# Kernel optimization log

Measured on AMD Instinct MI355X. Metric: run time of the kernel, lower is better.

The kernel has to match this reference:

```python
import jax, jax.numpy as jnp
import numpy as np

DIM = 192
HEADS = 6
HEAD_DIM = DIM // HEADS
WS = (7, 7, 7)
SHIFT = (3, 3, 3)
RES = (14, 56, 56)
MLP_HIDDEN = DIM * 4
N = WS[0] * WS[1] * WS[2]  # 343 tokens per window
SCALE = HEAD_DIM ** (-0.5)


def _rel_pos_index():
    coords = np.stack(np.meshgrid(np.arange(WS[0]), np.arange(WS[1]), np.arange(WS[2]), indexing='ij'))
    cf = coords.reshape(3, -1)  # (3, N)
    rel = (cf[:, :, None] - cf[:, None, :]).transpose(1, 2, 0).astype(np.int64)  # (N, N, 3)
    rel[..., 0] += WS[0] - 1
    rel[..., 1] += WS[1] - 1
    rel[..., 2] += WS[2] - 1
    rel[..., 0] *= (2 * WS[1] - 1) * (2 * WS[2] - 1)
    rel[..., 1] *= 2 * WS[2] - 1
    return rel.sum(-1)  # (N, N)


def _attn_mask():
    S, H, W = RES
    img = np.zeros((S, H, W), dtype=np.float32)
    cnt = 0
    for s in (slice(0, -WS[0]), slice(-WS[0], -SHIFT[0]), slice(-SHIFT[0], None)):
        for h in (slice(0, -WS[1]), slice(-WS[1], -SHIFT[1]), slice(-SHIFT[1], None)):
            for w in (slice(0, -WS[2]), slice(-WS[2], -SHIFT[2]), slice(-SHIFT[2], None)):
                img[s, h, w] = cnt
                cnt += 1
    m = img.reshape(S // WS[0], WS[0], H // WS[1], WS[1], W // WS[2], WS[2])
    m = m.transpose(0, 2, 4, 1, 3, 5).reshape(-1, N)  # (nW, N)
    diff = m[:, None, :] - m[:, :, None]
    return np.where(diff != 0, -100.0, 0.0).astype(np.float32)  # (nW, N, N)


REL_IDX = jnp.asarray(_rel_pos_index())
ATTN_MASK = jnp.asarray(_attn_mask())


def _window_partition(x):
    # x: (B, S, H, W, C) -> (B*nW, N, C)
    B, S, H, W, C = x.shape
    x = x.reshape(B, S // WS[0], WS[0], H // WS[1], WS[1], W // WS[2], WS[2], C)
    x = x.transpose(0, 1, 3, 5, 2, 4, 6, 7)
    return x.reshape(-1, N, C)


def _window_reverse(wins, B):
    S, H, W = RES
    C = wins.shape[-1]
    x = wins.reshape(B, S // WS[0], H // WS[1], W // WS[2], WS[0], WS[1], WS[2], C)
    x = x.transpose(0, 1, 4, 2, 5, 3, 6, 7)
    return x.reshape(B, S, H, W, C)


def _layernorm(x, g, b):
    mu = x.mean(-1, keepdims=True)
    var = ((x - mu) ** 2).mean(-1, keepdims=True)
    return (x - mu) * jax.lax.rsqrt(var + 1e-5) * g + b


def setup_inputs() -> dict:
    key = jax.random.key(0)
    ks = jax.random.split(key, 16)
    p = lambda k, shape, s=0.02: (jax.random.normal(k, shape, dtype=jnp.float32) * s)
    return {
        'x': jax.random.normal(ks[0], (1, DIM) + RES, dtype=jnp.float32),
        'norm1_g': jnp.ones((DIM,), jnp.float32),
        'norm1_b': jnp.zeros((DIM,), jnp.float32),
        'qkv_w': p(ks[1], (DIM, 3 * DIM)),
        'qkv_b': jnp.zeros((3 * DIM,), jnp.float32),
        'rpb_table': p(ks[2], ((2 * WS[0] - 1) * (2 * WS[1] - 1) * (2 * WS[2] - 1), HEADS)),
        'proj_w': p(ks[3], (DIM, DIM)),
        'proj_b': jnp.zeros((DIM,), jnp.float32),
        'norm2_g': jnp.ones((DIM,), jnp.float32),
        'norm2_b': jnp.zeros((DIM,), jnp.float32),
        'fc1_w': p(ks[4], (DIM, MLP_HIDDEN)),
        'fc1_b': jnp.zeros((MLP_HIDDEN,), jnp.float32),
        'fc2_w': p(ks[5], (MLP_HIDDEN, DIM)),
        'fc2_b': jnp.zeros((DIM,), jnp.float32),
    }


def reference(x, norm1_g, norm1_b, qkv_w, qkv_b, rpb_table, proj_w, proj_b,
              norm2_g, norm2_b, fc1_w, fc1_b, fc2_w, fc2_b):
    B, C, S, H, W = x.shape
    L = S * H * W
    xt = x.transpose(0, 2, 3, 4, 1).reshape(B, L, C)  # b (s h w) c
    shortcut = xt
    xn = _layernorm(xt, norm1_g, norm1_b).reshape(B, S, H, W, C)
    xs = jnp.roll(xn, (-SHIFT[0], -SHIFT[1], -SHIFT[2]), axis=(1, 2, 3))
    xw = _window_partition(xs)  # (B*nW, N, C)
    B_ = xw.shape[0]
    nW = B_ // B

    qkv = (xw @ qkv_w + qkv_b).reshape(B_, N, 3, HEADS, HEAD_DIM)
    q = qkv[:, :, 0].transpose(0, 2, 1, 3) * SCALE  # (B_, h, N, d)
    k = qkv[:, :, 1].transpose(0, 2, 1, 3)
    v = qkv[:, :, 2].transpose(0, 2, 1, 3)

    attn = jnp.einsum('bhnd,bhmd->bhnm', q, k)
    bias = rpb_table[REL_IDX.reshape(-1)].reshape(N, N, HEADS).transpose(2, 0, 1)  # (h, N, N)
    attn = attn + bias[None]
    attn = attn.reshape(B, nW, HEADS, N, N) + ATTN_MASK[None, :, None]
    attn = jax.nn.softmax(attn.reshape(B_, HEADS, N, N), axis=-1)

    out = jnp.einsum('bhnm,bhmd->bhnd', attn, v).transpose(0, 2, 1, 3).reshape(B_, N, C)
    out = out @ proj_w + proj_b

    xr = _window_reverse(out, B)
    xr = jnp.roll(xr, (SHIFT[0], SHIFT[1], SHIFT[2]), axis=(1, 2, 3)).reshape(B, L, C)
    xt = shortcut + xr

    h = _layernorm(xt, norm2_g, norm2_b)
    h = jax.nn.gelu(h @ fc1_w + fc1_b, approximate=False) @ fc2_w + fc2_b
    xt = xt + h

    return xt.reshape(B, S, H, W, C).transpose(0, 4, 1, 2, 3)  # (B, C, S, H, W)
```

## Files before the change

kernel.cpp:

```cpp
#include <hip/hip_runtime.h>
#include <hip/hip_bf16.h>
#include <math.h>

#define L_TOK 43904
#define NWIN 128
#define NTOK 343
#define NHEAD 6
#define SCALE 0.17677669529663687f
#define LOG2E 1.4426950408889634f
#define NMASK -144.26950408889634f
#define BSTRIDE 352
#define FIXMAX 16.0f

typedef __attribute__((ext_vector_type(8))) short short8;
typedef __attribute__((ext_vector_type(4))) float f32x4;

__device__ __forceinline__ unsigned short f2bf(float x) {
    union { float f; unsigned int u; } v; v.f = x;
    unsigned int r = v.u + 0x7fffu + ((v.u >> 16) & 1u);
    return (unsigned short)(r >> 16);
}
__device__ __forceinline__ unsigned int cvtpk(float a, float b) {
    unsigned int r;
    asm volatile("v_cvt_pk_bf16_f32 %0, %1, %2" : "=v"(r) : "v"(a), "v"(b));
    return r;
}
__device__ __forceinline__ void gload16(const void* g, void* l) {
    __builtin_amdgcn_global_load_lds((const __attribute__((address_space(1))) void*)g,
                                     (__attribute__((address_space(3))) void*)l, 16, 0, 0);
}

__device__ __forceinline__ int winrow(int l) {
    int s = l / 3136;
    int rem = l - s * 3136;
    int h = rem / 56;
    int w = rem - h * 56;
    int ps = s + 11; if (ps >= 14) ps -= 14;
    int ph = h + 53; if (ph >= 56) ph -= 56;
    int pw = w + 53; if (pw >= 56) pw -= 56;
    int wi = ((ps / 7) * 8 + ph / 7) * 8 + pw / 7;
    int tk = ((ps % 7) * 7 + ph % 7) * 7 + pw % 7;
    return wi * NTOK + tk;
}

__global__ __launch_bounds__(256) void convert_weights(
    const float* __restrict__ qkv_w, const float* __restrict__ qkv_b,
    const float* __restrict__ proj_w, const float* __restrict__ fc1_w,
    const float* __restrict__ fc2_w,
    unsigned short* __restrict__ qkvT, unsigned short* __restrict__ projT,
    unsigned short* __restrict__ fc1T, unsigned short* __restrict__ fc2T,
    float* __restrict__ qkvb_s) {
    int stride = gridDim.x * 256;
    int t0 = blockIdx.x * 256 + threadIdx.x;
    const float qs = SCALE * LOG2E;
    for (int i = t0; i < 576 * 192; i += stride) {
        int n = i / 192, k = i - n * 192;
        float v = qkv_w[k * 576 + n];
        if (n < 192) v *= qs;
        qkvT[i] = f2bf(v);
    }
    for (int i = t0; i < 192 * 192; i += stride) {
        int n = i / 192, k = i - n * 192;
        projT[i] = f2bf(proj_w[k * 192 + n]);
    }
    for (int i = t0; i < 768 * 192; i += stride) {
        int n = i / 192, k = i - n * 192;
        fc1T[i] = f2bf(fc1_w[k * 768 + n]);
    }
    for (int i = t0; i < 192 * 768; i += stride) {
        int n = i / 768, k = i - n * 768;
        fc2T[i] = f2bf(fc2_w[k * 192 + n]);
    }
    for (int i = t0; i < 576; i += stride) {
        float v = qkv_b[i]; if (i < 192) v *= qs;
        qkvb_s[i] = v;
    }
}

__global__ __launch_bounds__(256) void bias_compact(const float* __restrict__ table, float* __restrict__ biasC) {
    int q = blockIdx.x;
    int qs = q / 49, qh = (q / 7) % 7, qw = q % 7;
    for (int k = threadIdx.x; k < BSTRIDE; k += 256) {
        if (k < NTOK) {
            int ks = k / 49, kh = (k / 7) % 7, kw = k % 7;
            int idx = ((qs - ks + 6) * 13 + (qh - kh + 6)) * 13 + (qw - kw + 6);
            #pragma unroll
            for (int h = 0; h < NHEAD; ++h)
                biasC[((size_t)h * NTOK + q) * BSTRIDE + k] = table[idx * 6 + h] * LOG2E - FIXMAX;
        } else {
            #pragma unroll
            for (int h = 0; h < NHEAD; ++h)
                biasC[((size_t)h * NTOK + q) * BSTRIDE + k] = -30000.f;
        }
    }
}

__global__ __launch_bounds__(256) void ln1_part(const float* __restrict__ x,
                                                const float* __restrict__ g, const float* __restrict__ b,
                                                float* __restrict__ xt, unsigned short* __restrict__ xw) {
    __shared__ float tile[192 * 65];
    __shared__ float red[4][64];
    __shared__ float red2[4][64];
    __shared__ float mu_s[64], rs_s[64];
    int l0 = blockIdx.x * 64;
    int tid = threadIdx.x;
    int j = tid & 63, c4 = tid >> 6;
    for (int cb = 0; cb < 192; cb += 4)
        tile[(cb + c4) * 65 + j] = x[(size_t)(cb + c4) * L_TOK + l0 + j];
    __syncthreads();
    float s = 0.f, ss = 0.f;
    for (int c = c4 * 48; c < c4 * 48 + 48; ++c) {
        float v = tile[c * 65 + j];
        s += v; ss += v * v;
    }
    red[c4][j] = s; red2[c4][j] = ss;
    __syncthreads();
    if (tid < 64) {
        float S = red[0][j] + red[1][j] + red[2][j] + red[3][j];
        float SS = red2[0][j] + red2[1][j] + red2[2][j] + red2[3][j];
        float mu = S * (1.f / 192.f);
        float var = SS * (1.f / 192.f) - mu * mu;
        mu_s[j] = mu;
        rs_s[j] = rsqrtf(var + 1e-5f);
    }
    __syncthreads();
    int wave = tid >> 6, lid = tid & 63;
    for (int t = wave; t < 64; t += 4) {
        int l = l0 + t;
        int r = winrow(l);
        float mu = mu_s[t], rs = rs_s[t];
        #pragma unroll
        for (int q = 0; q < 3; ++q) {
            int c = q * 64 + lid;
            float v = tile[c * 65 + t];
            xt[(size_t)l * 192 + c] = v;
            xw[(size_t)r * 192 + c] = f2bf((v - mu) * rs * g[c] + b[c]);
        }
    }
}

template<int EPI, int OUTMODE>
__global__ __launch_bounds__(256, 3) void gemm_bf16(
    const unsigned short* __restrict__ A, const unsigned short* __restrict__ Bt,
    const float* __restrict__ bias, void* __restrict__ Cout,
    const float* __restrict__ xt, int N, int K) {
    __shared__ unsigned char smem[49152];
    unsigned short* sh = (unsigned short*)smem;
    const int tid = threadIdx.x;
    const int m0 = blockIdx.y * 128;
    const int n0 = blockIdx.x * 64;
    const int lane = tid & 63, wv = tid >> 6;
    const int wm = wv >> 1, wn = wv & 1;
    const int lr = lane & 15, lg = lane >> 4;
    const int KT = K >> 6;

    f32x4 acc[4][2];
    #pragma unroll
    for (int i = 0; i < 4; ++i)
        #pragma unroll
        for (int jj = 0; jj < 2; ++jj)
            acc[i][jj] = (f32x4){0.f, 0.f, 0.f, 0.f};

    #define STAGE(BUF, K0) { \
        unsigned short* dst = sh + (BUF) * 12288; \
        _Pragma("unroll") \
        for (int i_ = 0; i_ < 4; ++i_) { \
            int g_ = (i_ * 4 + wv) * 64 + lane; \
            int row_ = g_ >> 3, gc_ = g_ & 7; \
            gload16(A + (size_t)(m0 + row_) * K + (K0) + ((gc_ ^ (row_ & 7)) << 3), dst + g_ * 8); \
        } \
        _Pragma("unroll") \
        for (int i_ = 0; i_ < 2; ++i_) { \
            int g_ = (i_ * 4 + wv) * 64 + lane; \
            int row_ = g_ >> 3, gc_ = g_ & 7; \
            gload16(Bt + (size_t)(n0 + row_) * K + (K0) + ((gc_ ^ (row_ & 7)) << 3), dst + 8192 + g_ * 8); \
        } }

    STAGE(0, 0);
    __syncthreads();
    for (int kt = 0; kt < KT; ++kt) {
        int buf = kt & 1;
        if (kt + 1 < KT) STAGE(buf ^ 1, (kt + 1) << 6);
        const unsigned short* sA = sh + buf * 12288;
        const unsigned short* sB = sA + 8192;
        #pragma unroll
        for (int kk = 0; kk < 2; ++kk) {
            short8 a[4], b[2];
            #pragma unroll
            for (int i = 0; i < 4; ++i) {
                int row = wm * 64 + i * 16 + lr;
                a[i] = *(const short8*)(sA + row * 64 + (((kk * 4 + lg) ^ (lr & 7)) << 3));
            }
            #pragma unroll
            for (int jj = 0; jj < 2; ++jj) {
                int row = wn * 32 + jj * 16 + lr;
                b[jj] = *(const short8*)(sB + row * 64 + (((kk * 4 + lg) ^ (lr & 7)) << 3));
            }
            #pragma unroll
            for (int i = 0; i < 4; ++i)
                #pragma unroll
                for (int jj = 0; jj < 2; ++jj)
                    acc[i][jj] = __builtin_amdgcn_mfma_f32_16x16x32_bf16(a[i], b[jj], acc[i][jj], 0, 0, 0);
        }
        __syncthreads();
    }
    #undef STAGE

    if (OUTMODE == 2) {
        float* Cs = (float*)smem;
        #pragma unroll
        for (int i = 0; i < 4; ++i)
            #pragma unroll
            for (int jj = 0; jj < 2; ++jj)
                #pragma unroll
                for (int r = 0; r < 4; ++r) {
                    int row = wm * 64 + i * 16 + lg * 4 + r;
                    int col = wn * 32 + jj * 16 + lr;
                    float v = acc[i][jj][r] + bias[n0 + col] + xt[(size_t)(m0 + row) * 192 + n0 + col];
                    Cs[row * 68 + col] = v;
                }
        __syncthreads();
        float* outp = (float*)Cout;
        int c = tid & 63;
        #pragma unroll
        for (int j4 = tid >> 6; j4 < 32; j4 += 4) {
            f32x4 v;
            #pragma unroll
            for (int t = 0; t < 4; ++t) v[t] = Cs[(j4 * 4 + t) * 68 + c];
            *(f32x4*)&outp[(size_t)(n0 + c) * L_TOK + m0 + j4 * 4] = v;
        }
    } else {
        float bia[2];
        bia[0] = bias[n0 + wn * 32 + lr];
        bia[1] = bias[n0 + wn * 32 + 16 + lr];
        #pragma unroll
        for (int i = 0; i < 4; ++i) {
            #pragma unroll
            for (int jj = 0; jj < 2; ++jj) {
                #pragma unroll
                for (int r = 0; r < 4; ++r) {
                    float v = acc[i][jj][r] + bia[jj];
                    if (EPI == 1) v = 0.5f * v * (1.f + erff(v * 0.70710678118654752f));
                    int row = m0 + wm * 64 + i * 16 + lg * 4 + r;
                    int col = n0 + wn * 32 + jj * 16 + lr;
                    if (OUTMODE == 1) ((float*)Cout)[(size_t)row * N + col] = v;
                    else ((unsigned short*)Cout)[(size_t)row * N + col] = f2bf(v);
                }
            }
        }
    }
}

__global__ __launch_bounds__(256) void gemm_proj_ln(
    const unsigned short* __restrict__ A, const unsigned short* __restrict__ Bt,
    const float* __restrict__ bias, const float* __restrict__ g2, const float* __restrict__ b2,
    float* __restrict__ xt, unsigned short* __restrict__ h1) {
    __shared__ unsigned short As[2][64 * 64];
    __shared__ unsigned short Bs[2][192 * 64];
    const int tid = threadIdx.x;
    const int m0 = blockIdx.x * 64;
    const int lane = tid & 63, wv = tid >> 6;
    const int lr = lane & 15, lg = lane >> 4;
    const int K = 192;

    f32x4 acc[12];
    #pragma unroll
    for (int jj = 0; jj < 12; ++jj) acc[jj] = (f32x4){0.f, 0.f, 0.f, 0.f};

    #define PSTAGE(BUF, K0) { \
        _Pragma("unroll") \
        for (int i_ = 0; i_ < 2; ++i_) { \
            int g_ = i_ * 256 + tid; \
            int row_ = g_ >> 3, gc_ = g_ & 7; \
            gload16(A + (size_t)(m0 + row_) * K + (K0) + ((gc_ ^ (row_ & 7)) << 3), &As[BUF][g_ * 8]); \
        } \
        _Pragma("unroll") \
        for (int i_ = 0; i_ < 6; ++i_) { \
            int g_ = i_ * 256 + tid; \
            int row_ = g_ >> 3, gc_ = g_ & 7; \
            gload16(Bt + (size_t)row_ * K + (K0) + ((gc_ ^ (row_ & 7)) << 3), &Bs[BUF][g_ * 8]); \
        } }

    PSTAGE(0, 0);
    __syncthreads();
    for (int kt = 0; kt < 3; ++kt) {
        int buf = kt & 1;
        if (kt + 1 < 3) PSTAGE(buf ^ 1, (kt + 1) << 6);
        #pragma unroll
        for (int kk = 0; kk < 2; ++kk) {
            int arow = wv * 16 + lr;
            short8 a = *(const short8*)(&As[buf][arow * 64 + (((kk * 4 + lg) ^ (lr & 7)) << 3)]);
            #pragma unroll
            for (int jj = 0; jj < 12; ++jj) {
                int brow = jj * 16 + lr;
                short8 b = *(const short8*)(&Bs[buf][brow * 64 + (((kk * 4 + lg) ^ (lr & 7)) << 3)]);
                acc[jj] = __builtin_amdgcn_mfma_f32_16x16x32_bf16(a, b, acc[jj], 0, 0, 0);
            }
        }
        __syncthreads();
    }
    #undef PSTAGE

    #pragma unroll
    for (int r = 0; r < 4; ++r) {
        int m = m0 + wv * 16 + lg * 4 + r;
        int wi = m / 343, tk = m - wi * 343;
        int ts = tk / 49, rm = tk - ts * 49, th = rm / 7, tw = rm - th * 7;
        int ps = (wi >> 6) * 7 + ts, ph = ((wi >> 3) & 7) * 7 + th, pw = (wi & 7) * 7 + tw;
        int ss_ = ps + 3; if (ss_ >= 14) ss_ -= 14;
        int hh = ph + 3; if (hh >= 56) hh -= 56;
        int ww = pw + 3; if (ww >= 56) ww -= 56;
        size_t l = ((size_t)ss_ * 56 + hh) * 56 + ww;
        float val[12];
        float sum = 0.f, ssum = 0.f;
        #pragma unroll
        for (int jj = 0; jj < 12; ++jj) {
            int col = jj * 16 + lr;
            float v = acc[jj][r] + bias[col] + xt[l * 192 + col];
            xt[l * 192 + col] = v;
            val[jj] = v; sum += v; ssum += v * v;
        }
        #pragma unroll
        for (int off = 1; off < 16; off <<= 1) {
            sum += __shfl_xor(sum, off);
            ssum += __shfl_xor(ssum, off);
        }
        float mu = sum * (1.f / 192.f);
        float rs = rsqrtf(ssum * (1.f / 192.f) - mu * mu + 1e-5f);
        #pragma unroll
        for (int jj = 0; jj < 12; ++jj) {
            int col = jj * 16 + lr;
            h1[l * 192 + col] = f2bf((val[jj] - mu) * rs * g2[col] + b2[col]);
        }
    }
}

__global__ __launch_bounds__(256) void attn_flash(
    const unsigned short* __restrict__ qkv, const float* __restrict__ biasC,
    unsigned short* __restrict__ aout) {
    __shared__ unsigned short Ks[352 * 32];
    __shared__ unsigned short Vt[32][360];
    __shared__ unsigned int Ps2[4][16][20];
    __shared__ unsigned char regq[352];
    const int w = blockIdx.x, h = blockIdx.y;
    const int tid = threadIdx.x;
    const size_t base = (size_t)w * NTOK * 576;

    for (int g = tid; g < 1372; g += 256) {
        int row = g >> 2, c = g & 3;
        gload16(qkv + base + (size_t)row * 576 + 192 + h * 32 + ((c ^ ((row >> 1) & 3)) << 3), Ks + g * 8);
    }
    if (tid < 36) {
        short8 z = {};
        *(short8*)(Ks + (343 + (tid >> 2)) * 32 + (tid & 3) * 8) = z;
    }
    for (int idx = tid; idx < 688; idx += 256) {
        int jp = idx >> 2, c = idx & 3;
        int j0 = jp * 2, j1 = j0 + 1;
        short8 v0 = *(const short8*)(qkv + base + (size_t)j0 * 576 + 384 + h * 32 + c * 8);
        short8 v1 = {};
        if (j1 < NTOK) v1 = *(const short8*)(qkv + base + (size_t)j1 * 576 + 384 + h * 32 + c * 8);
        #pragma unroll
        for (int i = 0; i < 8; ++i) {
            ushort2 pr; pr.x = (unsigned short)v0[i]; pr.y = (unsigned short)v1[i];
            *(ushort2*)&Vt[c * 8 + i][j0] = pr;
        }
    }
    for (int idx = tid; idx < 128; idx += 256) {
        ushort2 z; z.x = 0; z.y = 0;
        *(ushort2*)&Vt[idx >> 2][344 + (idx & 3) * 2] = z;
    }
    {
        const int wis = w >> 6, wih = (w >> 3) & 7, wiw = w & 7;
        for (int n = tid; n < 352; n += 256) {
            unsigned char rv = 0;
            if (n < NTOK) {
                int ts = n / 49, r49 = n - ts * 49, th = r49 / 7, tw = r49 - th * 7;
                int ps = wis * 7 + ts, ph = wih * 7 + th, pw = wiw * 7 + tw;
                int rs = ps < 7 ? 0 : (ps < 11 ? 1 : 2);
                int rh = ph < 49 ? 0 : (ph < 53 ? 1 : 2);
                int rw = pw < 49 ? 0 : (pw < 53 ? 1 : 2);
                rv = (unsigned char)(rs * 9 + rh * 3 + rw);
            }
            regq[n] = rv;
        }
    }
    __syncthreads();

    const int wid = tid >> 6, l = tid & 63, lr = l & 15, lg = l >> 4;
    const int kchunk = (lg ^ ((lr >> 1) & 3)) << 3;

    for (int qt = wid; qt < 22; qt += 4) {
        int qrow = qt * 16 + lr;
        int qr = qrow < NTOK ? qrow : NTOK - 1;
        short8 qa = *(const short8*)(qkv + base + (size_t)qr * 576 + h * 32 + lg * 8);
        unsigned int rq = regq[qr];
        const float* bq = biasC + ((size_t)h * NTOK + qr) * BSTRIDE + lg * 4;

        float lsum = 0.f;
        f32x4 o0 = (f32x4){0.f, 0.f, 0.f, 0.f};
        f32x4 o1 = (f32x4){0.f, 0.f, 0.f, 0.f};
        const f32x4 zv = (f32x4){0.f, 0.f, 0.f, 0.f};

        #pragma unroll 1
        for (int kb = 0; kb < 11; ++kb) {
            const int kt0 = 2 * kb, kt1 = 2 * kb + 1;
            short8 k0 = *(const short8*)(Ks + (kt0 * 16 + lr) * 32 + kchunk);
            short8 k1 = *(const short8*)(Ks + (kt1 * 16 + lr) * 32 + kchunk);
            f32x4 s0 = __builtin_amdgcn_mfma_f32_16x16x32_bf16(k0, qa, zv, 0, 0, 0);
            f32x4 s1 = __builtin_amdgcn_mfma_f32_16x16x32_bf16(k1, qa, zv, 0, 0, 0);
            f32x4 bv0 = *(const f32x4*)(bq + kt0 * 16);
            f32x4 bv1 = *(const f32x4*)(bq + kt1 * 16);
            unsigned int rb0 = *(const unsigned int*)&regq[kt0 * 16 + lg * 4];
            unsigned int rb1 = *(const unsigned int*)&regq[kt1 * 16 + lg * 4];
            f32x4 p0, p1;
            #pragma unroll
            for (int r = 0; r < 4; ++r) {
                float m0 = (((rb0 >> (r * 8)) & 255u) != rq) ? NMASK : 0.f;
                float m1 = (((rb1 >> (r * 8)) & 255u) != rq) ? NMASK : 0.f;
                p0[r] = exp2f(s0[r] + bv0[r] + m0);
                p1[r] = exp2f(s1[r] + bv1[r] + m1);
                lsum += p0[r] + p1[r];
            }
            Ps2[wid][lr][lg * 2 + 0] = cvtpk(p0[0], p0[1]);
            Ps2[wid][lr][lg * 2 + 1] = cvtpk(p0[2], p0[3]);
            Ps2[wid][lr][8 + lg * 2 + 0] = cvtpk(p1[0], p1[1]);
            Ps2[wid][lr][8 + lg * 2 + 1] = cvtpk(p1[2], p1[3]);
            short8 pa = *(const short8*)&Ps2[wid][lr][lg * 4];
            short8 v0 = *(const short8*)&Vt[lr][kb * 32 + lg * 8];
            short8 v1 = *(const short8*)&Vt[16 + lr][kb * 32 + lg * 8];
            o0 = __builtin_amdgcn_mfma_f32_16x16x32_bf16(pa, v0, o0, 0, 0, 0);
            o1 = __builtin_amdgcn_mfma_f32_16x16x32_bf16(pa, v1, o1, 0, 0, 0);
        }
        lsum += __shfl_xor(lsum, 16);
        lsum += __shfl_xor(lsum, 32);
        float inv = 1.f / lsum;

        #pragma unroll
        for (int r = 0; r < 4; ++r) {
            float iv = __shfl(inv, lg * 4 + r);
            int q = qt * 16 + lg * 4 + r;
            if (q < NTOK) {
                size_t orow = ((size_t)w * NTOK + q) * 192 + h * 32;
                aout[orow + lr] = f2bf(o0[r] * iv);
                aout[orow + 16 + lr] = f2bf(o1[r] * iv);
            }
        }
    }
}

extern "C" void kernel_launch(void* const* d_in, const int* in_sizes, int n_in,
                              void* d_out, int out_size, void* d_ws, size_t ws_size,
                              hipStream_t stream) {
    const float* x      = (const float*)d_in[0];
    const float* n1g    = (const float*)d_in[1];
    const float* n1b    = (const float*)d_in[2];
    const float* qkv_w  = (const float*)d_in[3];
    const float* qkv_b  = (const float*)d_in[4];
    const float* rpb    = (const float*)d_in[5];
    const float* proj_w = (const float*)d_in[6];
    const float* proj_b = (const float*)d_in[7];
    const float* n2g    = (const float*)d_in[8];
    const float* n2b    = (const float*)d_in[9];
    const float* fc1_w  = (const float*)d_in[10];
    const float* fc1_b  = (const float*)d_in[11];
    const float* fc2_w  = (const float*)d_in[12];
    const float* fc2_b  = (const float*)d_in[13];
    float* out = (float*)d_out;

    char* p = (char*)d_ws;
    float* xt = (float*)p;                     p += (size_t)L_TOK * 192 * 4;
    unsigned short* xw = (unsigned short*)p;
    unsigned short* h1 = xw;                   p += (size_t)L_TOK * 192 * 2;
    unsigned short* qkvb = (unsigned short*)p;
    unsigned short* h2 = qkvb;                 p += (size_t)L_TOK * 768 * 2;
    unsigned short* aoutb = (unsigned short*)p; p += (size_t)L_TOK * 192 * 2;
    float* biasC = (float*)p;                  p += (size_t)NHEAD * NTOK * BSTRIDE * 4 + 256;
    unsigned short* qkvT = (unsigned short*)p; p += (size_t)576 * 192 * 2;
    unsigned short* projT = (unsigned short*)p; p += (size_t)192 * 192 * 2;
    unsigned short* fc1T = (unsigned short*)p; p += (size_t)768 * 192 * 2;
    unsigned short* fc2T = (unsigned short*)p; p += (size_t)192 * 768 * 2;
    float* qkvb_s = (float*)p;                 p += 576 * 4;

    convert_weights<<<576, 256, 0, stream>>>(qkv_w, qkv_b, proj_w, fc1_w, fc2_w,
                                             qkvT, projT, fc1T, fc2T, qkvb_s);
    bias_compact<<<343, 256, 0, stream>>>(rpb, biasC);
    ln1_part<<<686, 256, 0, stream>>>(x, n1g, n1b, xt, xw);
    gemm_bf16<0, 0><<<dim3(9, 343), 256, 0, stream>>>(xw, qkvT, qkvb_s, qkvb, nullptr, 576, 192);
    attn_flash<<<dim3(NWIN, NHEAD), 256, 0, stream>>>(qkvb, biasC, aoutb);
    gemm_proj_ln<<<686, 256, 0, stream>>>(aoutb, projT, proj_b, n2g, n2b, xt, h1);
    gemm_bf16<1, 0><<<dim3(12, 343), 256, 0, stream>>>(h1, fc1T, fc1_b, h2, nullptr, 768, 192);
    gemm_bf16<0, 2><<<dim3(3, 343), 256, 0, stream>>>(h2, fc2T, fc2_b, out, xt, 192, 768);
}
```

Baseline: 223.5 us.

## Fuse MLP fc1+GELU+fc2 into one kernel keeping hidden activations on-chip

Replaces the separate fc1 (with GELU) and fc2 GEMM launches with a single mlp_fused kernel. Each block loads 64 rows of the normalized input into LDS, computes the hidden layer in 64-column chunks, applies GELU, stages each chunk in LDS and accumulates it directly into the fc2 output, then adds the bias and residual and writes the transposed output. This removes the round trip of the 768-wide bf16 hidden tensor through global memory. In exchange, weights are read directly from global memory per wave without LDS staging, each wave only covers 16 rows, and the grid has just 686 blocks, so MFMA utilization may fall.

```diff
diff --git a/kernel.cpp b/kernel.cpp
--- a/kernel.cpp
+++ b/kernel.cpp
@@ -139,11 +139,9 @@
     }
 }
 
-template<int EPI, int OUTMODE>
 __global__ __launch_bounds__(256, 3) void gemm_bf16(
     const unsigned short* __restrict__ A, const unsigned short* __restrict__ Bt,
-    const float* __restrict__ bias, void* __restrict__ Cout,
-    const float* __restrict__ xt, int N, int K) {
+    const float* __restrict__ bias, unsigned short* __restrict__ Cout, int N, int K) {
     __shared__ unsigned char smem[49152];
     unsigned short* sh = (unsigned short*)smem;
     const int tid = threadIdx.x;
@@ -206,46 +204,18 @@
     }
     #undef STAGE
 
-    if (OUTMODE == 2) {
-        float* Cs = (float*)smem;
-        #pragma unroll
-        for (int i = 0; i < 4; ++i)
-            #pragma unroll
-            for (int jj = 0; jj < 2; ++jj)
-                #pragma unroll
-                for (int r = 0; r < 4; ++r) {
-                    int row = wm * 64 + i * 16 + lg * 4 + r;
-                    int col = wn * 32 + jj * 16 + lr;
-                    float v = acc[i][jj][r] + bias[n0 + col] + xt[(size_t)(m0 + row) * 192 + n0 + col];
-                    Cs[row * 68 + col] = v;
-                }
-        __syncthreads();
-        float* outp = (float*)Cout;
-        int c = tid & 63;
-        #pragma unroll
-        for (int j4 = tid >> 6; j4 < 32; j4 += 4) {
-            f32x4 v;
-            #pragma unroll
-            for (int t = 0; t < 4; ++t) v[t] = Cs[(j4 * 4 + t) * 68 + c];
-            *(f32x4*)&outp[(size_t)(n0 + c) * L_TOK + m0 + j4 * 4] = v;
-        }
-    } else {
-        float bia[2];
-        bia[0] = bias[n0 + wn * 32 + lr];
-        bia[1] = bias[n0 + wn * 32 + 16 + lr];
-        #pragma unroll
-        for (int i = 0; i < 4; ++i) {
-            #pragma unroll
-            for (int jj = 0; jj < 2; ++jj) {
-                #pragma unroll
-                for (int r = 0; r < 4; ++r) {
-                    float v = acc[i][jj][r] + bia[jj];
-                    if (EPI == 1) v = 0.5f * v * (1.f + erff(v * 0.70710678118654752f));
-                    int row = m0 + wm * 64 + i * 16 + lg * 4 + r;
-                    int col = n0 + wn * 32 + jj * 16 + lr;
-                    if (OUTMODE == 1) ((float*)Cout)[(size_t)row * N + col] = v;
-                    else ((unsigned short*)Cout)[(size_t)row * N + col] = f2bf(v);
-                }
+    float bia[2];
+    bia[0] = bias[n0 + wn * 32 + lr];
+    bia[1] = bias[n0 + wn * 32 + 16 + lr];
+    #pragma unroll
+    for (int i = 0; i < 4; ++i) {
+        #pragma unroll
+        for (int jj = 0; jj < 2; ++jj) {
+            #pragma unroll
+            for (int r = 0; r < 4; ++r) {
+                int row = m0 + wm * 64 + i * 16 + lg * 4 + r;
+                int col = n0 + wn * 32 + jj * 16 + lr;
+                Cout[(size_t)row * N + col] = f2bf(acc[i][jj][r] + bia[jj]);
             }
         }
     }
@@ -332,6 +302,100 @@
             int col = jj * 16 + lr;
             h1[l * 192 + col] = f2bf((val[jj] - mu) * rs * g2[col] + b2[col]);
         }
+    }
+}
+
+__global__ __launch_bounds__(256) void mlp_fused(
+    const unsigned short* __restrict__ A,
+    const unsigned short* __restrict__ W1,
+    const float* __restrict__ b1,
+    const unsigned short* __restrict__ W2,
+    const float* __restrict__ b2,
+    const float* __restrict__ xt,
+    float* __restrict__ out) {
+    __shared__ unsigned short A_s[64 * 192];
+    __shared__ unsigned short h_s[4][16][72];
+    const int tid = threadIdx.x;
+    const int m0 = blockIdx.x * 64;
+    const int lane = tid & 63, wv = tid >> 6;
+    const int lr = lane & 15, lg = lane >> 4;
+
+    #pragma unroll
+    for (int i = 0; i < 6; ++i) {
+        int g = i * 256 + tid;
+        int row = g / 24, gc = g - row * 24;
+        gload16(A + (size_t)(m0 + row) * 192 + ((gc ^ (row & 7)) << 3), A_s + g * 8);
+    }
+    __syncthreads();
+
+    f32x4 acc2[12];
+    #pragma unroll
+    for (int j = 0; j < 12; ++j) acc2[j] = (f32x4){0.f, 0.f, 0.f, 0.f};
+
+    const unsigned short* Arow = A_s + (wv * 16 + lr) * 192;
+    const int asw = lr & 7;
+
+    #pragma unroll 1
+    for (int hc = 0; hc < 12; ++hc) {
+        f32x4 acc1[4];
+        #pragma unroll
+        for (int j = 0; j < 4; ++j) acc1[j] = (f32x4){0.f, 0.f, 0.f, 0.f};
+        #pragma unroll
+        for (int kt = 0; kt < 6; ++kt) {
+            short8 a = *(const short8*)(Arow + (((kt * 4 + lg) ^ asw) << 3));
+            #pragma unroll
+            for (int jj = 0; jj < 4; ++jj) {
+                short8 b = *(const short8*)(W1 + (size_t)(hc * 64 + jj * 16 + lr) * 192 + kt * 32 + lg * 8);
+                acc1[jj] = __builtin_amdgcn_mfma_f32_16x16x32_bf16(a, b, acc1[jj], 0, 0, 0);
+            }
+        }
+        #pragma unroll
+        for (int jj = 0; jj < 4; ++jj) {
+            float bb = b1[hc * 64 + jj * 16 + lr];
+            #pragma unroll
+            for (int r = 0; r < 4; ++r) {
+                float v = acc1[jj][r] + bb;
+                v = 0.5f * v * (1.f + erff(v * 0.70710678118654752f));
+                h_s[wv][lg * 4 + r][jj * 16 + lr] = f2bf(v);
+            }
+        }
+        __syncthreads();
+        #pragma unroll
+        for (int k0 = 0; k0 < 2; ++k0) {
+            short8 hf = *(const short8*)(&h_s[wv][lr][k0 * 32 + lg * 8]);
+            #pragma unroll
+            for (int j2 = 0; j2 < 12; ++j2) {
+                short8 b = *(const short8*)(W2 + (size_t)(j2 * 16 + lr) * 768 + hc * 64 + k0 * 32 + lg * 8);
+                acc2[j2] = __builtin_amdgcn_mfma_f32_16x16x32_bf16(hf, b, acc2[j2], 0, 0, 0);
+            }
+        }
+        __syncthreads();
+    }
+
+    float* Cs = (float*)A_s;
+    #pragma unroll
+    for (int g = 0; g < 3; ++g) {
+        #pragma unroll
+        for (int jq = 0; jq < 4; ++jq) {
+            int j2 = g * 4 + jq;
+            int col = j2 * 16 + lr;
+            #pragma unroll
+            for (int r = 0; r < 4; ++r) {
+                int row = wv * 16 + lg * 4 + r;
+                float v = acc2[j2][r] + b2[col] + xt[(size_t)(m0 + row) * 192 + col];
+                Cs[row * 68 + jq * 16 + lr] = v;
+            }
+        }
+        __syncthreads();
+        int cl = tid & 63;
+        #pragma unroll
+        for (int j4 = tid >> 6; j4 < 16; j4 += 4) {
+            f32x4 v;
+            #pragma unroll
+            for (int t = 0; t < 4; ++t) v[t] = Cs[(j4 * 4 + t) * 68 + cl];
+            *(f32x4*)&out[(size_t)(g * 64 + cl) * L_TOK + m0 + j4 * 4] = v;
+        }
+        __syncthreads();
     }
 }
 
@@ -472,8 +536,7 @@
     float* xt = (float*)p;                     p += (size_t)L_TOK * 192 * 4;
     unsigned short* xw = (unsigned short*)p;
     unsigned short* h1 = xw;                   p += (size_t)L_TOK * 192 * 2;
-    unsigned short* qkvb = (unsigned short*)p;
-    unsigned short* h2 = qkvb;                 p += (size_t)L_TOK * 768 * 2;
+    unsigned short* qkvb = (unsigned short*)p; p += (size_t)L_TOK * 768 * 2;
     unsigned short* aoutb = (unsigned short*)p; p += (size_t)L_TOK * 192 * 2;
     float* biasC = (float*)p;                  p += (size_t)NHEAD * NTOK * BSTRIDE * 4 + 256;
     unsigned short* qkvT = (unsigned short*)p; p += (size_t)576 * 192 * 2;
@@ -486,9 +549,8 @@
                                              qkvT, projT, fc1T, fc2T, qkvb_s);
     bias_compact<<<343, 256, 0, stream>>>(rpb, biasC);
     ln1_part<<<686, 256, 0, stream>>>(x, n1g, n1b, xt, xw);
-    gemm_bf16<0, 0><<<dim3(9, 343), 256, 0, stream>>>(xw, qkvT, qkvb_s, qkvb, nullptr, 576, 192);
+    gemm_bf16<<<dim3(9, 343), 256, 0, stream>>>(xw, qkvT, qkvb_s, qkvb, 576, 192);
     attn_flash<<<dim3(NWIN, NHEAD), 256, 0, stream>>>(qkvb, biasC, aoutb);
     gemm_proj_ln<<<686, 256, 0, stream>>>(aoutb, projT, proj_b, n2g, n2b, xt, h1);
-    gemm_bf16<1, 0><<<dim3(12, 343), 256, 0, stream>>>(h1, fc1T, fc1_b, h2, nullptr, 768, 192);
-    gemm_bf16<0, 2><<<dim3(3, 343), 256, 0, stream>>>(h2, fc2T, fc2_b, out, xt, 192, 768);
-}
+    mlp_fused<<<686, 256, 0, stream>>>(h1, fc1T, fc1_b, fc2T, fc2_b, xt, out);
+}
```

Result: slower. 406.0 us (+81.6%).
